# Optimization experiments

Measured on AMD Instinct MI355X. Metric: run time of the kernel, lower is better.

## Reference

```python
import jax, jax.numpy as jnp
import numpy as np

B, W, H, V, L = 64, 512, 1024, 32000, 2


def setup_inputs() -> dict:
    key = jax.random.key(0)
    ks = jax.random.split(key, 20)
    s = 0.02  # init scale
    n = lambda k, shp: jax.random.normal(k, shp, jnp.float32)
    return {
        "input": jax.random.randint(ks[0], (B, 1), 0, V),
        "h0": n(ks[1], (L, B, H)),
        "c0": n(ks[2], (L, B, H)),
        "encoder_output": n(ks[3], (B, W, H)),
        "embedding": n(ks[4], (V, H)) * s,
        "W_ih0": n(ks[5], (4 * H, H)) * s,
        "W_hh0": n(ks[6], (4 * H, H)) * s,
        "b_ih0": n(ks[7], (4 * H,)) * s,
        "b_hh0": n(ks[8], (4 * H,)) * s,
        "W_ih1": n(ks[9], (4 * H, H)) * s,
        "W_hh1": n(ks[10], (4 * H, H)) * s,
        "b_ih1": n(ks[11], (4 * H,)) * s,
        "b_hh1": n(ks[12], (4 * H,)) * s,
        "att_w": n(ks[13], (2 * H,)) * s,
        "att_b": n(ks[14], (1,)) * s,
        "input_W": n(ks[15], (H, 2 * H)) * s,
        "input_b": n(ks[16], (H,)) * s,
        "out_W": n(ks[17], (V, H)) * s,
        "out_b": n(ks[18], (V,)) * s,
    }


def _lstm_step(x, h, c, W_ih, W_hh, b_ih, b_hh):
    # PyTorch gate order: i, f, g, o
    g = x @ W_ih.T + h @ W_hh.T + b_ih + b_hh
    i, f, gg, o = jnp.split(g, 4, axis=-1)
    c2 = jax.nn.sigmoid(f) * c + jax.nn.sigmoid(i) * jnp.tanh(gg)
    return jax.nn.sigmoid(o) * jnp.tanh(c2), c2


def reference(input, h0, c0, encoder_output, embedding,
              W_ih0, W_hh0, b_ih0, b_hh0, W_ih1, W_hh1, b_ih1, b_hh1,
              att_w, att_b, input_W, input_b, out_W, out_b):
    Hd = h0.shape[-1]
    emb = embedding[input]                       # (B,1,H)
    att_state = h0[-1] * c0[-1]                  # (B,H)
    # Vectorized replacement of the per-word cat+linear loop:
    # att_line(cat(enc_w, att_state)) = enc_w @ w_enc + att_state @ w_st + b
    w_enc, w_st = att_w[:Hd], att_w[Hd:]
    scores = encoder_output @ w_enc + (att_state @ w_st)[:, None] + att_b[0]  # (B,W)
    # Original quirk: weigth starts with a zeros column, then softmax over
    # weigth[:, 0:-1] -> zero column + scores for words 0..W-2 (last dropped).
    zeros = jnp.zeros((scores.shape[0], 1), scores.dtype)
    full = jnp.concatenate([zeros, scores[:, :-1]], axis=1)  # (B,W)
    wts = jax.nn.softmax(full, axis=1)
    ctx = jnp.einsum('bw,bwh->bh', wts, encoder_output)      # (B,H)
    x = jnp.concatenate([ctx, emb[:, 0, :]], axis=-1)        # (B,2H)
    x = x @ input_W.T + input_b                              # (B,H)
    h1, c1 = _lstm_step(x, h0[0], c0[0], W_ih0, W_hh0, b_ih0, b_hh0)
    h2, c2 = _lstm_step(h1, h0[1], c0[1], W_ih1, W_hh1, b_ih1, b_hh1)
    logits = h2 @ out_W.T + out_b                            # (B,V)
    logp = jax.nn.log_softmax(logits, axis=-1)[:, None, :]   # (B,1,V)
    return logp, jnp.stack([h1, h2]), jnp.stack([c1, c2])
```

## Files before the change

kernel.cpp:

```cpp
#include <hip/hip_runtime.h>
#include <hip/hip_bf16.h>

#define Bsz 64
#define Wln 512
#define Hd  1024
#define Vc  32000

typedef short v8s __attribute__((ext_vector_type(8)));
typedef float f32x4 __attribute__((ext_vector_type(4)));

__device__ inline unsigned short f2b(float f) {
  union { float f; unsigned u; } v; v.f = f;
  return (unsigned short)((v.u + 0x8000u) >> 16);
}
__device__ inline float wave_sum(float v) {
  #pragma unroll
  for (int o = 32; o; o >>= 1) v += __shfl_down(v, o);
  return v;
}
__device__ inline float wave_max(float v) {
  #pragma unroll
  for (int o = 32; o; o >>= 1) v = fmaxf(v, __shfl_down(v, o));
  return v;
}
__device__ inline float sigm(float x) { return 1.f / (1.f + expf(-x)); }

__device__ inline v8s cvt_frag(float4 x0, float4 x1) {
  v8s r;
  r[0] = (short)f2b(x0.x); r[1] = (short)f2b(x0.y);
  r[2] = (short)f2b(x0.z); r[3] = (short)f2b(x0.w);
  r[4] = (short)f2b(x1.x); r[5] = (short)f2b(x1.y);
  r[6] = (short)f2b(x1.z); r[7] = (short)f2b(x1.w);
  return r;
}

__device__ inline void stage_A(const float* __restrict__ A, int sA,
                               char* pool, int tid) {
  #pragma unroll
  for (int it = 0; it < 16; ++it) {
    int idx = it * 512 + tid;
    int row = idx >> 7, ch = idx & 127;
    const float* src = A + (size_t)row * sA + ch * 8;
    float4 x0 = *(const float4*)src;
    float4 x1 = *(const float4*)(src + 4);
    *(v8s*)(pool + row * 2048 + ((ch * 16) ^ ((row & 7) << 4))) = cvt_frag(x0, x1);
  }
}

__global__ __launch_bounds__(256) void k_scores_satt(
    const float* __restrict__ enc, const float* __restrict__ att_w,
    const float* __restrict__ h0, const float* __restrict__ c0,
    const float* __restrict__ att_b, const int* __restrict__ input,
    const float* __restrict__ emb,
    float* __restrict__ scores, float* __restrict__ s_att,
    float* __restrict__ cat)
{
  __shared__ float red[4];
  int t = threadIdx.x;
  if (blockIdx.x < 8192) {
    int row = blockIdx.x * 4 + (t >> 6);
    int lane = t & 63;
    const float* p = enc + (size_t)row * Hd + lane * 16;
    const float* w = att_w + lane * 16;
    float s = 0.f;
    #pragma unroll
    for (int c = 0; c < 4; ++c) {
      float4 e = *(const float4*)(p + c * 4);
      float4 ww = *(const float4*)(w + c * 4);
      s += e.x * ww.x + e.y * ww.y + e.z * ww.z + e.w * ww.w;
    }
    s = wave_sum(s);
    if (lane == 0) scores[row] = s;
  } else {
    int b = blockIdx.x - 8192;
    int idx = input[b];
    for (int j = t; j < Hd; j += 256)
      cat[b * 2 * Hd + Hd + j] = emb[(size_t)idx * Hd + j];
    size_t base = (size_t)(Bsz + b) * Hd;
    float s = 0.f;
    for (int j = t; j < Hd; j += 256)
      s += h0[base + j] * c0[base + j] * att_w[Hd + j];
    s = wave_sum(s);
    if ((t & 63) == 0) red[t >> 6] = s;
    __syncthreads();
    if (t == 0) s_att[b] = red[0] + red[1] + red[2] + red[3] + att_b[0];
  }
}

__global__ __launch_bounds__(512) void k_ctx(
    const float* __restrict__ scores, const float* __restrict__ s_att,
    const float* __restrict__ enc, float* __restrict__ cat)
{
  __shared__ float w_sh[Wln];
  __shared__ float part[8][256];
  __shared__ float redA[8], redB[8];
  int b = blockIdx.x >> 2, qtr = blockIdx.x & 3;
  int tid = threadIdx.x, w = tid >> 6, lane = tid & 63;
  float sa = s_att[b];
  const float* sr = scores + b * Wln;
  float v = (tid == 0) ? 0.f : sr[tid - 1] + sa;
  float m = wave_max(v);
  if (lane == 0) redA[w] = m;
  __syncthreads();
  float M = redA[0];
  #pragma unroll
  for (int i = 1; i < 8; ++i) M = fmaxf(M, redA[i]);
  float e = expf(v - M);
  float s = wave_sum(e);
  if (lane == 0) redB[w] = s;
  __syncthreads();
  float S = redB[0];
  #pragma unroll
  for (int i = 1; i < 8; ++i) S += redB[i];
  w_sh[tid] = e / S;
  __syncthreads();

  const float* pb = enc + (size_t)b * Wln * Hd + qtr * 256 + lane * 4;
  float a0 = 0, a1 = 0, a2 = 0, a3 = 0;
  #pragma unroll 4
  for (int i = 0; i < 64; ++i) {
    int row = w * 64 + i;
    float4 ev = *(const float4*)(pb + (size_t)row * Hd);
    float wi = w_sh[row];
    a0 += wi * ev.x; a1 += wi * ev.y; a2 += wi * ev.z; a3 += wi * ev.w;
  }
  part[w][lane * 4 + 0] = a0; part[w][lane * 4 + 1] = a1;
  part[w][lane * 4 + 2] = a2; part[w][lane * 4 + 3] = a3;
  __syncthreads();
  if (tid < 256) {
    float s2 = 0.f;
    #pragma unroll
    for (int ww = 0; ww < 8; ++ww) s2 += part[ww][tid];
    cat[b * 2 * Hd + qtr * 256 + tid] = s2;
  }
}

__global__ __launch_bounds__(512) void k_input_gemm(
    const float* __restrict__ cat, const float* __restrict__ inW,
    const float* __restrict__ inb, float* __restrict__ x)
{
  __shared__ __align__(16) char pool[131072];
  const int tid = threadIdx.x;
  const int w = tid >> 6, lane = tid & 63;
  const int r = lane & 15, q = lane >> 4;
  const int kh = w;
  const int n0 = blockIdx.x * 16;

  f32x4 acc[4] = {{0,0,0,0},{0,0,0,0},{0,0,0,0},{0,0,0,0}};
  #pragma unroll
  for (int p = 0; p < 2; ++p) {
    const float* bp = inW + (size_t)(n0 + r) * 2048 + p * 1024 + kh * 128 + q * 8;
    float4 breg[4][2];
    #pragma unroll
    for (int kk = 0; kk < 4; ++kk) {
      breg[kk][0] = *(const float4*)(bp + kk * 32);
      breg[kk][1] = *(const float4*)(bp + kk * 32 + 4);
    }
    stage_A(cat + p * 1024, 2048, pool, tid);
    __syncthreads();
    const int swz = (r & 7) << 4;
    #pragma unroll
    for (int kk = 0; kk < 4; ++kk) {
      v8s bf = cvt_frag(breg[kk][0], breg[kk][1]);
      int cb = ((kh * 128 + kk * 32 + q * 8) * 2) ^ swz;
      #pragma unroll
      for (int m = 0; m < 4; ++m) {
        v8s af = *(const v8s*)(pool + (m * 16 + r) * 2048 + cb);
        acc[m] = __builtin_amdgcn_mfma_f32_16x16x32_bf16(af, bf, acc[m], 0, 0, 0);
      }
    }
    __syncthreads();
  }

  float (*red)[64][17] = (float(*)[64][17])pool;
  #pragma unroll
  for (int m = 0; m < 4; ++m)
    #pragma unroll
    for (int rr = 0; rr < 4; ++rr)
      red[w][lane][m * 4 + rr] = acc[m][rr];
  __syncthreads();

  #pragma unroll
  for (int it = 0; it < 2; ++it) {
    int e = it * 512 + tid;
    int cc = e & 15, rowi = e >> 4;
    int idx = ((rowi >> 4) << 2) + (rowi & 3);
    int le  = (((rowi >> 2) & 3) << 4) + cc;
    float s = 0.f;
    #pragma unroll
    for (int j = 0; j < 8; ++j) s += red[j][le][idx];
    x[(size_t)rowi * Hd + n0 + cc] = s + inb[n0 + cc];
  }
}

__global__ __launch_bounds__(512) void k_gate_lstm(
    const float* __restrict__ xA, const float* __restrict__ hA,
    const float* __restrict__ W_ih, const float* __restrict__ W_hh,
    const float* __restrict__ b_ih, const float* __restrict__ b_hh,
    const float* __restrict__ c0,
    float* __restrict__ out_h, float* __restrict__ out_c)
{
  __shared__ __align__(16) char pool[131072];
  const int tid = threadIdx.x;
  const int w = tid >> 6, lane = tid & 63;
  const int r = lane & 15, q = lane >> 4;
  const int nsub = w & 1, kh = w >> 1;
  const int cc_w = nsub * 16 + r;
  const int gate = cc_w >> 3, jl = cc_w & 7;
  const size_t Brow = (size_t)(gate * Hd + blockIdx.x * 8 + jl);

  f32x4 acc[4] = {{0,0,0,0},{0,0,0,0},{0,0,0,0},{0,0,0,0}};
  const float* Amat[2] = { xA, hA };
  const float* Wmat[2] = { W_ih, W_hh };
  #pragma unroll
  for (int p = 0; p < 2; ++p) {
    const float* bp = Wmat[p] + Brow * Hd + kh * 256 + q * 8;
    float4 breg[8][2];
    #pragma unroll
    for (int kk = 0; kk < 8; ++kk) {
      breg[kk][0] = *(const float4*)(bp + kk * 32);
      breg[kk][1] = *(const float4*)(bp + kk * 32 + 4);
    }
    stage_A(Amat[p], Hd, pool, tid);
    __syncthreads();
    const int swz = (r & 7) << 4;
    #pragma unroll
    for (int kk = 0; kk < 8; ++kk) {
      v8s bf = cvt_frag(breg[kk][0], breg[kk][1]);
      int cb = ((kh * 256 + kk * 32 + q * 8) * 2) ^ swz;
      #pragma unroll
      for (int m = 0; m < 4; ++m) {
        v8s af = *(const v8s*)(pool + (m * 16 + r) * 2048 + cb);
        acc[m] = __builtin_amdgcn_mfma_f32_16x16x32_bf16(af, bf, acc[m], 0, 0, 0);
      }
    }
    __syncthreads();
  }

  float (*red)[64][17] = (float(*)[64][17])pool;
  #pragma unroll
  for (int m = 0; m < 4; ++m)
    #pragma unroll
    for (int rr = 0; rr < 4; ++rr)
      red[w][lane][m * 4 + rr] = acc[m][rr];
  __syncthreads();

  int b = tid >> 3, jl2 = tid & 7;
  int jg = blockIdx.x * 8 + jl2;
  float gv[4];
  #pragma unroll
  for (int g2 = 0; g2 < 4; ++g2) {
    int cc = g2 * 8 + jl2;
    int ns2 = cc >> 4, lo = cc & 15;
    int idx = ((b >> 4) << 2) + (b & 3);
    int le  = (((b >> 2) & 3) << 4) + lo;
    float s = 0.f;
    #pragma unroll
    for (int j = 0; j < 4; ++j) s += red[ns2 + j * 2][le][idx];
    gv[g2] = s + b_ih[g2 * Hd + jg] + b_hh[g2 * Hd + jg];
  }
  float c = sigm(gv[1]) * c0[(size_t)b * Hd + jg] + sigm(gv[0]) * tanhf(gv[2]);
  float h = sigm(gv[3]) * tanhf(c);
  out_h[(size_t)b * Hd + jg] = h;
  out_c[(size_t)b * Hd + jg] = c;
}

__global__ __launch_bounds__(512) void k_logits(
    const float* __restrict__ A, const float* __restrict__ B,
    const float* __restrict__ bias, float* __restrict__ out)
{
  __shared__ __align__(16) char pool[131072];
  const int tid = threadIdx.x;
  const int w = tid >> 6, lane = tid & 63;
  const int r = lane & 15, q = lane >> 4;
  const int nsub = w & 3, kh = w >> 2;
  const int n0 = blockIdx.x * 64;

  const float* bp = B + (size_t)(n0 + nsub * 16 + r) * Hd + kh * 512 + q * 8;
  float4 breg[16][2];
  #pragma unroll
  for (int kk = 0; kk < 16; ++kk) {
    breg[kk][0] = *(const float4*)(bp + kk * 32);
    breg[kk][1] = *(const float4*)(bp + kk * 32 + 4);
  }
  stage_A(A, Hd, pool, tid);
  __syncthreads();

  f32x4 acc[4] = {{0,0,0,0},{0,0,0,0},{0,0,0,0},{0,0,0,0}};
  const int swz = (r & 7) << 4;
  #pragma unroll
  for (int kk = 0; kk < 16; ++kk) {
    v8s bf = cvt_frag(breg[kk][0], breg[kk][1]);
    int cb = ((kh * 512 + kk * 32 + q * 8) * 2) ^ swz;
    #pragma unroll
    for (int m = 0; m < 4; ++m) {
      v8s af = *(const v8s*)(pool + (m * 16 + r) * 2048 + cb);
      acc[m] = __builtin_amdgcn_mfma_f32_16x16x32_bf16(af, bf, acc[m], 0, 0, 0);
    }
  }
  __syncthreads();

  float (*red)[64][17] = (float(*)[64][17])pool;
  #pragma unroll
  for (int m = 0; m < 4; ++m)
    #pragma unroll
    for (int rr = 0; rr < 4; ++rr)
      red[w][lane][m * 4 + rr] = acc[m][rr];
  __syncthreads();

  #pragma unroll
  for (int it = 0; it < 8; ++it) {
    int e = it * 512 + tid;
    int cc = e & 63, rowi = e >> 6;
    int ns2 = cc >> 4, lo = cc & 15;
    int idx = ((rowi >> 4) << 2) + (rowi & 3);
    int le  = (((rowi >> 2) & 3) << 4) + lo;
    float s = red[ns2][le][idx] + red[ns2 + 4][le][idx];
    out[(size_t)rowi * Vc + n0 + cc] = s + bias[n0 + cc];
  }
}

__global__ __launch_bounds__(512) void k_lsm_part(
    const float* __restrict__ lg, float* __restrict__ pm, float* __restrict__ ps)
{
  __shared__ float redA[8], redB[8];
  int b = blockIdx.x >> 2, qc = blockIdx.x & 3;
  int tid = threadIdx.x, w = tid >> 6, lane = tid & 63;
  const float* row = lg + (size_t)b * Vc + qc * 8000;
  float m = -1e30f;
  for (int j = tid * 4; j < 8000; j += 2048) {
    float4 v = *(const float4*)(row + j);
    m = fmaxf(m, fmaxf(fmaxf(v.x, v.y), fmaxf(v.z, v.w)));
  }
  m = wave_max(m);
  if (lane == 0) redA[w] = m;
  __syncthreads();
  float M = redA[0];
  #pragma unroll
  for (int i = 1; i < 8; ++i) M = fmaxf(M, redA[i]);
  float s = 0.f;
  for (int j = tid * 4; j < 8000; j += 2048) {
    float4 v = *(const float4*)(row + j);
    s += expf(v.x - M) + expf(v.y - M) + expf(v.z - M) + expf(v.w - M);
  }
  s = wave_sum(s);
  if (lane == 0) redB[w] = s;
  __syncthreads();
  if (tid == 0) {
    float S = redB[0];
    #pragma unroll
    for (int i = 1; i < 8; ++i) S += redB[i];
    pm[blockIdx.x] = M; ps[blockIdx.x] = S;
  }
}

__global__ __launch_bounds__(512) void k_lsm_sub(
    float* __restrict__ lg, const float* __restrict__ pm, const float* __restrict__ ps)
{
  int b = blockIdx.x >> 2, qc = blockIdx.x & 3;
  int tid = threadIdx.x;
  float M = pm[b * 4];
  #pragma unroll
  for (int i = 1; i < 4; ++i) M = fmaxf(M, pm[b * 4 + i]);
  float S = 0.f;
  #pragma unroll
  for (int i = 0; i < 4; ++i) S += ps[b * 4 + i] * expf(pm[b * 4 + i] - M);
  float lse = M + logf(S);
  float* row = lg + (size_t)b * Vc + qc * 8000;
  for (int j = tid * 4; j < 8000; j += 2048) {
    float4 v = *(const float4*)(row + j);
    v.x -= lse; v.y -= lse; v.z -= lse; v.w -= lse;
    *(float4*)(row + j) = v;
  }
}

extern "C" void kernel_launch(void* const* d_in, const int* in_sizes, int n_in,
                              void* d_out, int out_size, void* d_ws, size_t ws_size,
                              hipStream_t stream)
{
  const int*   input = (const int*)d_in[0];
  const float* h0    = (const float*)d_in[1];
  const float* c0    = (const float*)d_in[2];
  const float* enc   = (const float*)d_in[3];
  const float* emb   = (const float*)d_in[4];
  const float* W_ih0 = (const float*)d_in[5];
  const float* W_hh0 = (const float*)d_in[6];
  const float* b_ih0 = (const float*)d_in[7];
  const float* b_hh0 = (const float*)d_in[8];
  const float* W_ih1 = (const float*)d_in[9];
  const float* W_hh1 = (const float*)d_in[10];
  const float* b_ih1 = (const float*)d_in[11];
  const float* b_hh1 = (const float*)d_in[12];
  const float* att_w = (const float*)d_in[13];
  const float* att_b = (const float*)d_in[14];
  const float* inW   = (const float*)d_in[15];
  const float* inb   = (const float*)d_in[16];
  const float* outW  = (const float*)d_in[17];
  const float* outb  = (const float*)d_in[18];
  float* out = (float*)d_out;

  char* ws = (char*)d_ws;
  float* cat    = (float*)(ws + 0);
  float* x      = (float*)(ws + 524288);
  float* scores = (float*)(ws + 786432);
  float* s_att  = (float*)(ws + 917504);
  float* pm     = (float*)(ws + 918528);
  float* ps     = (float*)(ws + 919552);

  float* out_h = out + (size_t)Bsz * Vc;
  float* out_c = out_h + 2 * Bsz * Hd;
  float* h1 = out_h;
  float* h2 = out_h + Bsz * Hd;

  k_scores_satt<<<8256, 256, 0, stream>>>(enc, att_w, h0, c0, att_b, input, emb,
                                          scores, s_att, cat);
  k_ctx<<<Bsz * 4, 512, 0, stream>>>(scores, s_att, enc, cat);
  k_input_gemm<<<64, 512, 0, stream>>>(cat, inW, inb, x);
  k_gate_lstm<<<128, 512, 0, stream>>>(x, h0, W_ih0, W_hh0, b_ih0, b_hh0,
                                       c0, h1, out_c);
  k_gate_lstm<<<128, 512, 0, stream>>>(h1, h0 + (size_t)Bsz * Hd, W_ih1, W_hh1,
                                       b_ih1, b_hh1, c0 + (size_t)Bsz * Hd,
                                       h2, out_c + Bsz * Hd);
  k_logits<<<500, 512, 0, stream>>>(h2, outW, outb, out);
  k_lsm_part<<<256, 512, 0, stream>>>(out, pm, ps);
  k_lsm_sub<<<256, 512, 0, stream>>>(out, pm, ps);
}
```

Baseline: 142.3 us.

## Split input GEMM over K, widen LSTM grid, fuse log-softmax partials into logits

The input projection is split into two K-halves run by separate blocks, and their partial outputs are summed while the first LSTM kernel stages its A operand. Both gate kernels now use 256 blocks with 4 hidden units each and an 8-way K split, which doubles parallelism across CUs. The logits kernel now computes per-row max and exp-sum partials for each 64-column tile with wave reductions, removing the separate pass that re-read the full logits. The costs are an extra x buffer, more partials to reduce in k_lsm_sub, and half the threads idle in the gate epilogue.

```diff
diff --git a/kernel.cpp b/kernel.cpp
--- a/kernel.cpp
+++ b/kernel.cpp
@@ -21,6 +21,16 @@
 __device__ inline float wave_max(float v) {
   #pragma unroll
   for (int o = 32; o; o >>= 1) v = fmaxf(v, __shfl_down(v, o));
+  return v;
+}
+__device__ inline float wave_sum_all(float v) {
+  #pragma unroll
+  for (int o = 32; o; o >>= 1) v += __shfl_xor(v, o);
+  return v;
+}
+__device__ inline float wave_max_all(float v) {
+  #pragma unroll
+  for (int o = 32; o; o >>= 1) v = fmaxf(v, __shfl_xor(v, o));
   return v;
 }
 __device__ inline float sigm(float x) { return 1.f / (1.f + expf(-x)); }
@@ -34,8 +44,8 @@
   return r;
 }
 
-__device__ inline void stage_A(const float* __restrict__ A, int sA,
-                               char* pool, int tid) {
+__device__ inline void stage_A(const float* __restrict__ A, const float* __restrict__ Ab,
+                               int sA, char* pool, int tid) {
   #pragma unroll
   for (int it = 0; it < 16; ++it) {
     int idx = it * 512 + tid;
@@ -43,6 +53,13 @@
     const float* src = A + (size_t)row * sA + ch * 8;
     float4 x0 = *(const float4*)src;
     float4 x1 = *(const float4*)(src + 4);
+    if (Ab) {
+      const float* s2 = Ab + (size_t)row * sA + ch * 8;
+      float4 y0 = *(const float4*)s2;
+      float4 y1 = *(const float4*)(s2 + 4);
+      x0.x += y0.x; x0.y += y0.y; x0.z += y0.z; x0.w += y0.w;
+      x1.x += y1.x; x1.y += y1.y; x1.z += y1.z; x1.w += y1.w;
+    }
     *(v8s*)(pool + row * 2048 + ((ch * 16) ^ ((row & 7) << 4))) = cvt_frag(x0, x1);
   }
 }
@@ -137,26 +154,95 @@
 
 __global__ __launch_bounds__(512) void k_input_gemm(
     const float* __restrict__ cat, const float* __restrict__ inW,
-    const float* __restrict__ inb, float* __restrict__ x)
+    const float* __restrict__ inb, float* __restrict__ x1, float* __restrict__ x2)
 {
   __shared__ __align__(16) char pool[131072];
   const int tid = threadIdx.x;
   const int w = tid >> 6, lane = tid & 63;
   const int r = lane & 15, q = lane >> 4;
   const int kh = w;
-  const int n0 = blockIdx.x * 16;
+  const int half = (blockIdx.x >= 64);
+  const int n0 = (blockIdx.x & 63) * 16;
+  const float* A = cat + half * 1024;
+  const float* B = inW + half * 1024;
+  float* out = half ? x2 : x1;
+
+  const float* bp = B + (size_t)(n0 + r) * 2048 + kh * 128 + q * 8;
+  float4 breg[4][2];
+  #pragma unroll
+  for (int kk = 0; kk < 4; ++kk) {
+    breg[kk][0] = *(const float4*)(bp + kk * 32);
+    breg[kk][1] = *(const float4*)(bp + kk * 32 + 4);
+  }
+  stage_A(A, nullptr, 2048, pool, tid);
+  __syncthreads();
 
   f32x4 acc[4] = {{0,0,0,0},{0,0,0,0},{0,0,0,0},{0,0,0,0}};
+  const int swz = (r & 7) << 4;
+  #pragma unroll
+  for (int kk = 0; kk < 4; ++kk) {
+    v8s bf = cvt_frag(breg[kk][0], breg[kk][1]);
+    int cb = ((kh * 128 + kk * 32 + q * 8) * 2) ^ swz;
+    #pragma unroll
+    for (int m = 0; m < 4; ++m) {
+      v8s af = *(const v8s*)(pool + (m * 16 + r) * 2048 + cb);
+      acc[m] = __builtin_amdgcn_mfma_f32_16x16x32_bf16(af, bf, acc[m], 0, 0, 0);
+    }
+  }
+  __syncthreads();
+
+  float (*red)[64][17] = (float(*)[64][17])pool;
+  #pragma unroll
+  for (int m = 0; m < 4; ++m)
+    #pragma unroll
+    for (int rr = 0; rr < 4; ++rr)
+      red[w][lane][m * 4 + rr] = acc[m][rr];
+  __syncthreads();
+
+  #pragma unroll
+  for (int it = 0; it < 2; ++it) {
+    int e = it * 512 + tid;
+    int cc = e & 15, rowi = e >> 4;
+    int idx = ((rowi >> 4) << 2) + (rowi & 3);
+    int le  = (((rowi >> 2) & 3) << 4) + cc;
+    float s = 0.f;
+    #pragma unroll
+    for (int j = 0; j < 8; ++j) s += red[j][le][idx];
+    float bb = half ? 0.f : inb[n0 + cc];
+    out[(size_t)rowi * Hd + n0 + cc] = s + bb;
+  }
+}
+
+__global__ __launch_bounds__(512) void k_gate_lstm(
+    const float* __restrict__ xA, const float* __restrict__ xAb,
+    const float* __restrict__ hA,
+    const float* __restrict__ W_ih, const float* __restrict__ W_hh,
+    const float* __restrict__ b_ih, const float* __restrict__ b_hh,
+    const float* __restrict__ c0,
+    float* __restrict__ out_h, float* __restrict__ out_c)
+{
+  __shared__ __align__(16) char pool[131072];
+  const int tid = threadIdx.x;
+  const int w = tid >> 6, lane = tid & 63;
+  const int r = lane & 15, q = lane >> 4;
+  const int kh = w;
+  const int gate = r >> 2, jl = r & 3;
+  const size_t Brow = (size_t)gate * Hd + blockIdx.x * 4 + jl;
+
+  f32x4 acc[4] = {{0,0,0,0},{0,0,0,0},{0,0,0,0},{0,0,0,0}};
+  const float* Amat[2] = { xA, hA };
+  const float* Abm[2]  = { xAb, nullptr };
+  const float* Wmat[2] = { W_ih, W_hh };
   #pragma unroll
   for (int p = 0; p < 2; ++p) {
-    const float* bp = inW + (size_t)(n0 + r) * 2048 + p * 1024 + kh * 128 + q * 8;
+    const float* bp = Wmat[p] + Brow * Hd + kh * 128 + q * 8;
     float4 breg[4][2];
     #pragma unroll
     for (int kk = 0; kk < 4; ++kk) {
       breg[kk][0] = *(const float4*)(bp + kk * 32);
       breg[kk][1] = *(const float4*)(bp + kk * 32 + 4);
     }
-    stage_A(cat + p * 1024, 2048, pool, tid);
+    stage_A(Amat[p], Abm[p], Hd, pool, tid);
     __syncthreads();
     const int swz = (r & 7) << 4;
     #pragma unroll
@@ -180,94 +266,31 @@
       red[w][lane][m * 4 + rr] = acc[m][rr];
   __syncthreads();
 
-  #pragma unroll
-  for (int it = 0; it < 2; ++it) {
-    int e = it * 512 + tid;
-    int cc = e & 15, rowi = e >> 4;
-    int idx = ((rowi >> 4) << 2) + (rowi & 3);
-    int le  = (((rowi >> 2) & 3) << 4) + cc;
-    float s = 0.f;
-    #pragma unroll
-    for (int j = 0; j < 8; ++j) s += red[j][le][idx];
-    x[(size_t)rowi * Hd + n0 + cc] = s + inb[n0 + cc];
-  }
-}
-
-__global__ __launch_bounds__(512) void k_gate_lstm(
-    const float* __restrict__ xA, const float* __restrict__ hA,
-    const float* __restrict__ W_ih, const float* __restrict__ W_hh,
-    const float* __restrict__ b_ih, const float* __restrict__ b_hh,
-    const float* __restrict__ c0,
-    float* __restrict__ out_h, float* __restrict__ out_c)
-{
-  __shared__ __align__(16) char pool[131072];
-  const int tid = threadIdx.x;
-  const int w = tid >> 6, lane = tid & 63;
-  const int r = lane & 15, q = lane >> 4;
-  const int nsub = w & 1, kh = w >> 1;
-  const int cc_w = nsub * 16 + r;
-  const int gate = cc_w >> 3, jl = cc_w & 7;
-  const size_t Brow = (size_t)(gate * Hd + blockIdx.x * 8 + jl);
-
-  f32x4 acc[4] = {{0,0,0,0},{0,0,0,0},{0,0,0,0},{0,0,0,0}};
-  const float* Amat[2] = { xA, hA };
-  const float* Wmat[2] = { W_ih, W_hh };
-  #pragma unroll
-  for (int p = 0; p < 2; ++p) {
-    const float* bp = Wmat[p] + Brow * Hd + kh * 256 + q * 8;
-    float4 breg[8][2];
-    #pragma unroll
-    for (int kk = 0; kk < 8; ++kk) {
-      breg[kk][0] = *(const float4*)(bp + kk * 32);
-      breg[kk][1] = *(const float4*)(bp + kk * 32 + 4);
-    }
-    stage_A(Amat[p], Hd, pool, tid);
-    __syncthreads();
-    const int swz = (r & 7) << 4;
-    #pragma unroll
-    for (int kk = 0; kk < 8; ++kk) {
-      v8s bf = cvt_frag(breg[kk][0], breg[kk][1]);
-      int cb = ((kh * 256 + kk * 32 + q * 8) * 2) ^ swz;
+  if (tid < 256) {
+    int b = tid >> 2, jl2 = tid & 3;
+    int jg = blockIdx.x * 4 + jl2;
+    float gv[4];
+    #pragma unroll
+    for (int g2 = 0; g2 < 4; ++g2) {
+      int cc = g2 * 4 + jl2;
+      int idx = ((b >> 4) << 2) + (b & 3);
+      int le  = (((b >> 2) & 3) << 4) + cc;
+      float s = 0.f;
       #pragma unroll
-      for (int m = 0; m < 4; ++m) {
-        v8s af = *(const v8s*)(pool + (m * 16 + r) * 2048 + cb);
-        acc[m] = __builtin_amdgcn_mfma_f32_16x16x32_bf16(af, bf, acc[m], 0, 0, 0);
-      }
-    }
-    __syncthreads();
-  }
-
-  float (*red)[64][17] = (float(*)[64][17])pool;
-  #pragma unroll
-  for (int m = 0; m < 4; ++m)
-    #pragma unroll
-    for (int rr = 0; rr < 4; ++rr)
-      red[w][lane][m * 4 + rr] = acc[m][rr];
-  __syncthreads();
-
-  int b = tid >> 3, jl2 = tid & 7;
-  int jg = blockIdx.x * 8 + jl2;
-  float gv[4];
-  #pragma unroll
-  for (int g2 = 0; g2 < 4; ++g2) {
-    int cc = g2 * 8 + jl2;
-    int ns2 = cc >> 4, lo = cc & 15;
-    int idx = ((b >> 4) << 2) + (b & 3);
-    int le  = (((b >> 2) & 3) << 4) + lo;
-    float s = 0.f;
-    #pragma unroll
-    for (int j = 0; j < 4; ++j) s += red[ns2 + j * 2][le][idx];
-    gv[g2] = s + b_ih[g2 * Hd + jg] + b_hh[g2 * Hd + jg];
-  }
-  float c = sigm(gv[1]) * c0[(size_t)b * Hd + jg] + sigm(gv[0]) * tanhf(gv[2]);
-  float h = sigm(gv[3]) * tanhf(c);
-  out_h[(size_t)b * Hd + jg] = h;
-  out_c[(size_t)b * Hd + jg] = c;
+      for (int j = 0; j < 8; ++j) s += red[j][le][idx];
+      gv[g2] = s + b_ih[(size_t)g2 * Hd + jg] + b_hh[(size_t)g2 * Hd + jg];
+    }
+    float c = sigm(gv[1]) * c0[(size_t)b * Hd + jg] + sigm(gv[0]) * tanhf(gv[2]);
+    float h = sigm(gv[3]) * tanhf(c);
+    out_h[(size_t)b * Hd + jg] = h;
+    out_c[(size_t)b * Hd + jg] = c;
+  }
 }
 
 __global__ __launch_bounds__(512) void k_logits(
     const float* __restrict__ A, const float* __restrict__ B,
-    const float* __restrict__ bias, float* __restrict__ out)
+    const float* __restrict__ bias, float* __restrict__ out,
+    float* __restrict__ pm, float* __restrict__ ps)
 {
   __shared__ __align__(16) char pool[131072];
   const int tid = threadIdx.x;
@@ -283,7 +306,7 @@
     breg[kk][0] = *(const float4*)(bp + kk * 32);
     breg[kk][1] = *(const float4*)(bp + kk * 32 + 4);
   }
-  stage_A(A, Hd, pool, tid);
+  stage_A(A, nullptr, Hd, pool, tid);
   __syncthreads();
 
   f32x4 acc[4] = {{0,0,0,0},{0,0,0,0},{0,0,0,0},{0,0,0,0}};
@@ -315,23 +338,22 @@
     int ns2 = cc >> 4, lo = cc & 15;
     int idx = ((rowi >> 4) << 2) + (rowi & 3);
     int le  = (((rowi >> 2) & 3) << 4) + lo;
-    float s = red[ns2][le][idx] + red[ns2 + 4][le][idx];
-    out[(size_t)rowi * Vc + n0 + cc] = s + bias[n0 + cc];
-  }
-}
-
-__global__ __launch_bounds__(512) void k_lsm_part(
-    const float* __restrict__ lg, float* __restrict__ pm, float* __restrict__ ps)
+    float val = red[ns2][le][idx] + red[ns2 + 4][le][idx] + bias[n0 + cc];
+    out[(size_t)rowi * Vc + n0 + cc] = val;
+    float wm = wave_max_all(val);
+    float we = wave_sum_all(expf(val - wm));
+    if (cc == 0) { pm[blockIdx.x * 64 + rowi] = wm; ps[blockIdx.x * 64 + rowi] = we; }
+  }
+}
+
+__global__ __launch_bounds__(512) void k_lsm_sub(
+    float* __restrict__ lg, const float* __restrict__ pm, const float* __restrict__ ps)
 {
   __shared__ float redA[8], redB[8];
   int b = blockIdx.x >> 2, qc = blockIdx.x & 3;
   int tid = threadIdx.x, w = tid >> 6, lane = tid & 63;
-  const float* row = lg + (size_t)b * Vc + qc * 8000;
   float m = -1e30f;
-  for (int j = tid * 4; j < 8000; j += 2048) {
-    float4 v = *(const float4*)(row + j);
-    m = fmaxf(m, fmaxf(fmaxf(v.x, v.y), fmaxf(v.z, v.w)));
-  }
+  for (int j = tid; j < 500; j += 512) m = fmaxf(m, pm[j * 64 + b]);
   m = wave_max(m);
   if (lane == 0) redA[w] = m;
   __syncthreads();
@@ -339,32 +361,13 @@
   #pragma unroll
   for (int i = 1; i < 8; ++i) M = fmaxf(M, redA[i]);
   float s = 0.f;
-  for (int j = tid * 4; j < 8000; j += 2048) {
-    float4 v = *(const float4*)(row + j);
-    s += expf(v.x - M) + expf(v.y - M) + expf(v.z - M) + expf(v.w - M);
-  }
+  for (int j = tid; j < 500; j += 512) s += ps[j * 64 + b] * expf(pm[j * 64 + b] - M);
   s = wave_sum(s);
   if (lane == 0) redB[w] = s;
   __syncthreads();
-  if (tid == 0) {
-    float S = redB[0];
-    #pragma unroll
-    for (int i = 1; i < 8; ++i) S += redB[i];
-    pm[blockIdx.x] = M; ps[blockIdx.x] = S;
-  }
-}
-
-__global__ __launch_bounds__(512) void k_lsm_sub(
-    float* __restrict__ lg, const float* __restrict__ pm, const float* __restrict__ ps)
-{
-  int b = blockIdx.x >> 2, qc = blockIdx.x & 3;
-  int tid = threadIdx.x;
-  float M = pm[b * 4];
-  #pragma unroll
-  for (int i = 1; i < 4; ++i) M = fmaxf(M, pm[b * 4 + i]);
-  float S = 0.f;
-  #pragma unroll
-  for (int i = 0; i < 4; ++i) S += ps[b * 4 + i] * expf(pm[b * 4 + i] - M);
+  float S = redB[0];
+  #pragma unroll
+  for (int i = 1; i < 8; ++i) S += redB[i];
   float lse = M + logf(S);
   float* row = lg + (size_t)b * Vc + qc * 8000;
   for (int j = tid * 4; j < 8000; j += 2048) {
@@ -401,11 +404,12 @@
 
   char* ws = (char*)d_ws;
   float* cat    = (float*)(ws + 0);
-  float* x      = (float*)(ws + 524288);
-  float* scores = (float*)(ws + 786432);
-  float* s_att  = (float*)(ws + 917504);
-  float* pm     = (float*)(ws + 918528);
-  float* ps     = (float*)(ws + 919552);
+  float* x1     = (float*)(ws + 524288);
+  float* x2     = (float*)(ws + 786432);
+  float* scores = (float*)(ws + 1048576);
+  float* s_att  = (float*)(ws + 1179648);
+  float* pm     = (float*)(ws + 1180672);
+  float* ps     = (float*)(ws + 1310720);
 
   float* out_h = out + (size_t)Bsz * Vc;
   float* out_c = out_h + 2 * Bsz * Hd;
@@ -415,13 +419,12 @@
   k_scores_satt<<<8256, 256, 0, stream>>>(enc, att_w, h0, c0, att_b, input, emb,
                                           scores, s_att, cat);
   k_ctx<<<Bsz * 4, 512, 0, stream>>>(scores, s_att, enc, cat);
-  k_input_gemm<<<64, 512, 0, stream>>>(cat, inW, inb, x);
-  k_gate_lstm<<<128, 512, 0, stream>>>(x, h0, W_ih0, W_hh0, b_ih0, b_hh0,
+  k_input_gemm<<<128, 512, 0, stream>>>(cat, inW, inb, x1, x2);
+  k_gate_lstm<<<256, 512, 0, stream>>>(x1, x2, h0, W_ih0, W_hh0, b_ih0, b_hh0,
                                        c0, h1, out_c);
-  k_gate_lstm<<<128, 512, 0, stream>>>(h1, h0 + (size_t)Bsz * Hd, W_ih1, W_hh1,
-                                       b_ih1, b_hh1, c0 + (size_t)Bsz * Hd,
-                                       h2, out_c + Bsz * Hd);
-  k_logits<<<500, 512, 0, stream>>>(h2, outW, outb, out);
-  k_lsm_part<<<256, 512, 0, stream>>>(out, pm, ps);
+  k_gate_lstm<<<256, 512, 0, stream>>>(h1, nullptr, h0 + (size_t)Bsz * Hd,
+                                       W_ih1, W_hh1, b_ih1, b_hh1,
+                                       c0 + (size_t)Bsz * Hd, h2, out_c + Bsz * Hd);
+  k_logits<<<500, 512, 0, stream>>>(h2, outW, outb, out, pm, ps);
   k_lsm_sub<<<256, 512, 0, stream>>>(out, pm, ps);
 }
```

Measured after the change: 143.7 us. No clear change (+1.0%).
